# Kernel optimization log

Hardware: AMD Instinct MI355X
Metric: run time of the kernel (lower is better)

## Reference

```python
import jax, jax.numpy as jnp
import numpy as np

HIDDEN = 128
IN = 28
OUT = 28


def _uniform(key, shape, fan_in):
    bound = 1.0 / np.sqrt(fan_in)
    return jax.random.uniform(key, shape, jnp.float32, -bound, bound)


def setup_inputs() -> dict:
    key = jax.random.key(0)
    ks = jax.random.split(key, 8)
    B, T = 4096, 256
    x = jax.random.normal(ks[0], (B, T, IN), jnp.float32)
    hidden = jnp.zeros((B, HIDDEN), jnp.float32)
    # torch nn.Linear default init: U(-1/sqrt(fan_in), 1/sqrt(fan_in))
    W_ih = _uniform(ks[1], (HIDDEN, IN), IN)
    b_ih = _uniform(ks[2], (HIDDEN,), IN)
    W_hh = _uniform(ks[3], (HIDDEN, HIDDEN), HIDDEN)
    b_hh = _uniform(ks[4], (HIDDEN,), HIDDEN)
    W_ho = _uniform(ks[5], (OUT * OUT, HIDDEN), HIDDEN)
    b_ho = _uniform(ks[6], (OUT * OUT,), HIDDEN)
    return {"x": x, "hidden": hidden, "W_ih": W_ih, "b_ih": b_ih,
            "W_hh": W_hh, "b_hh": b_hh, "W_ho": W_ho, "b_ho": b_ho}


def reference(x, hidden, W_ih, b_ih, W_hh, b_hh, W_ho, b_ho):
    # x: [B, T, IN]; hidden: [B, HIDDEN]
    def step(h, x_t):
        h = jax.nn.relu(x_t @ W_ih.T + b_ih + h @ W_hh.T + b_hh)
        return h, None

    # scan over time (leading axis) — equivalent to the python loop,
    # and only the final hidden feeds the output projection (the torch
    # code overwrites `output` every step, so only the last one matters).
    h_final, _ = jax.lax.scan(step, hidden, jnp.swapaxes(x, 0, 1))
    out = (h_final @ W_ho.T + b_ho).reshape(-1, OUT, OUT)  # [B, 28, 28]
    return out, h_final
```

## Files before the change

### kernel.cpp

```cpp
#include <hip/hip_runtime.h>
#include <hip/hip_bf16.h>

#define B_TOT   4096
#define T_STEPS 256
#define IN_D    28
#define HID     128
#define OUT_D   784
#define BM      16

typedef __bf16 bf16x8 __attribute__((ext_vector_type(8)));
typedef __bf16 bf16x4 __attribute__((ext_vector_type(4)));
typedef float  f32x4  __attribute__((ext_vector_type(4)));
typedef float  f32x2  __attribute__((ext_vector_type(2)));

__device__ __forceinline__ float bf2f(__bf16 b) {
    unsigned short s = __builtin_bit_cast(unsigned short, b);
    unsigned int u = ((unsigned int)s) << 16;
    return __builtin_bit_cast(float, u);
}
__device__ __forceinline__ unsigned short f2bfbits(float f) {
    unsigned int u = __builtin_bit_cast(unsigned int, f);
    u += 0x7fffu + ((u >> 16) & 1u);
    return (unsigned short)(u >> 16);
}

__device__ __forceinline__ int hswz(int row, int byteInRow) {
    return row * 256 + (byteInRow ^ ((row & 7) << 4));
}

#define BARLDS() asm volatile("s_waitcnt lgkmcnt(0)\n\ts_barrier" ::: "memory")

__global__ __launch_bounds__(512) void rnn_fused(
    const float* __restrict__ x,
    const float* __restrict__ h0,
    const float* __restrict__ W_ih,
    const float* __restrict__ b_ih,
    const float* __restrict__ W_hh,
    const float* __restrict__ b_hh,
    const float* __restrict__ W_ho,
    const float* __restrict__ b_ho,
    float* __restrict__ out)
{
    __shared__ __align__(16) unsigned char Hb[2][BM * 256];
    __shared__ __align__(16) unsigned char Xs[8 * BM * 256];

    const int tid  = threadIdx.x;
    const int lane = tid & 63;
    const int wv   = tid >> 6;
    const int ln15 = lane & 15;
    const int lg   = lane >> 4;
    const int b0   = blockIdx.x * BM;

    const int nt0 = wv * 16;
    bf16x8 bw[4];
    #pragma unroll
    for (int kc = 0; kc < 4; ++kc) {
        const float* p = W_hh + (nt0 + ln15) * HID + kc * 32 + lg * 8;
        bf16x8 v;
        #pragma unroll
        for (int e = 0; e < 8; ++e) v[e] = (__bf16)p[e];
        bw[kc] = v;
    }
    const __bf16 bzero = (__bf16)0.0f;
    bf16x8 bxf;
    {
        int n = nt0 + ln15;
        #pragma unroll
        for (int e = 0; e < 8; ++e) {
            int k = lg * 8 + e;
            bxf[e] = (k < IN_D) ? (__bf16)W_ih[n * IN_D + k] : bzero;
        }
    }
    f32x4 bias4;
    {
        int n = nt0 + 4 * lg;
        f32x4 bi = *(const f32x4*)(b_ih + n);
        f32x4 bh = *(const f32x4*)(b_hh + n);
        bias4 = bi + bh;
    }

    if (tid < 256) {
        int row = tid >> 4, cg = tid & 15;
        const float* p = h0 + (size_t)(b0 + row) * HID + cg * 8;
        bf16x8 hv;
        #pragma unroll
        for (int e = 0; e < 8; ++e) hv[e] = (__bf16)p[e];
        *(bf16x8*)(&Hb[0][hswz(row, cg * 16)]) = hv;
    }
    if (tid < 256) {
        int slot = tid >> 5, idx = tid & 31, row = idx >> 1, d = idx & 1;
        *(unsigned int*)(&Xs[slot * (BM * 256) + hswz(row, 56 + d * 4)]) = 0u;
    }
    const int xrow = tid / 14, xpair = tid % 14;
    const bool xthr = (tid < 224);
    const float* xbase = x + (size_t)(b0 + xrow) * T_STEPS * IN_D + xpair * 2;
    if (xthr) {
        #pragma unroll
        for (int s = 0; s < 4; ++s) {
            f32x2 v = *(const f32x2*)(xbase + (size_t)s * IN_D);
            unsigned int pk = ((unsigned int)f2bfbits(v[1]) << 16) | f2bfbits(v[0]);
            *(unsigned int*)(&Xs[s * (BM * 256) + hswz(xrow, xpair * 4)]) = pk;
        }
    }
    f32x2 sx0 = {0.f, 0.f}, sx1 = sx0, sx2 = sx0, sx3 = sx0;
    __syncthreads();

#define STEP(T, STGL, STGW)                                                     \
    {                                                                           \
        const int rb = (T) & 1;                                                 \
        STGL                                                                    \
        bf16x8 ax  = *(const bf16x8*)(&Xs[((T) & 7) * (BM * 256) + hswz(ln15, lg * 16)]); \
        bf16x8 ah0 = *(const bf16x8*)(&Hb[rb][hswz(ln15,   0 + lg * 16)]);      \
        bf16x8 ah1 = *(const bf16x8*)(&Hb[rb][hswz(ln15,  64 + lg * 16)]);      \
        bf16x8 ah2 = *(const bf16x8*)(&Hb[rb][hswz(ln15, 128 + lg * 16)]);      \
        bf16x8 ah3 = *(const bf16x8*)(&Hb[rb][hswz(ln15, 192 + lg * 16)]);      \
        f32x4 zz = {0.f, 0.f, 0.f, 0.f};                                        \
        f32x4 a = __builtin_amdgcn_mfma_f32_16x16x32_bf16(bxf,   ax,  bias4, 0, 0, 0); \
        f32x4 c = __builtin_amdgcn_mfma_f32_16x16x32_bf16(bw[1], ah1, zz, 0, 0, 0); \
        a = __builtin_amdgcn_mfma_f32_16x16x32_bf16(bw[0], ah0, a, 0, 0, 0);    \
        c = __builtin_amdgcn_mfma_f32_16x16x32_bf16(bw[3], ah3, c, 0, 0, 0);    \
        a = __builtin_amdgcn_mfma_f32_16x16x32_bf16(bw[2], ah2, a, 0, 0, 0);    \
        f32x4 s = a + c;                                                        \
        bf16x4 w;                                                               \
        _Pragma("unroll")                                                       \
        for (int r = 0; r < 4; ++r) {                                           \
            float v = s[r];                                                     \
            w[r] = (__bf16)(v > 0.f ? v : 0.f);                                 \
        }                                                                       \
        *(bf16x4*)(&Hb[rb ^ 1][hswz(ln15, nt0 * 2 + lg * 8)]) = w;              \
        STGW                                                                    \
        BARLDS();                                                               \
    }

#define STG_LOAD(T)                                                             \
        if (((T) + 4 < T_STEPS) && xthr) {                                      \
            sx0 = *(const f32x2*)(xbase + (size_t)((T) + 4) * IN_D);            \
            sx1 = *(const f32x2*)(xbase + (size_t)((T) + 5) * IN_D);            \
            sx2 = *(const f32x2*)(xbase + (size_t)((T) + 6) * IN_D);            \
            sx3 = *(const f32x2*)(xbase + (size_t)((T) + 7) * IN_D);            \
        }
#define STG_WRITE(T)                                                            \
        if (((T) + 4 < T_STEPS) && xthr) {                                      \
            unsigned int p0 = ((unsigned int)f2bfbits(sx0[1]) << 16) | f2bfbits(sx0[0]); \
            unsigned int p1 = ((unsigned int)f2bfbits(sx1[1]) << 16) | f2bfbits(sx1[0]); \
            unsigned int p2 = ((unsigned int)f2bfbits(sx2[1]) << 16) | f2bfbits(sx2[0]); \
            unsigned int p3 = ((unsigned int)f2bfbits(sx3[1]) << 16) | f2bfbits(sx3[0]); \
            *(unsigned int*)(&Xs[(((T) + 4) & 7) * (BM * 256) + hswz(xrow, xpair * 4)]) = p0; \
            *(unsigned int*)(&Xs[(((T) + 5) & 7) * (BM * 256) + hswz(xrow, xpair * 4)]) = p1; \
            *(unsigned int*)(&Xs[(((T) + 6) & 7) * (BM * 256) + hswz(xrow, xpair * 4)]) = p2; \
            *(unsigned int*)(&Xs[(((T) + 7) & 7) * (BM * 256) + hswz(xrow, xpair * 4)]) = p3; \
        }

    for (int t = 0; t < T_STEPS; t += 8) {
        STEP(t + 0, STG_LOAD(t + 0), )
        STEP(t + 1, , )
        STEP(t + 2, , STG_WRITE(t + 0))
        STEP(t + 3, , )
        STEP(t + 4, STG_LOAD(t + 4), )
        STEP(t + 5, , )
        STEP(t + 6, , STG_WRITE(t + 4))
        STEP(t + 7, , )
    }
#undef STEP
#undef STG_LOAD
#undef STG_WRITE

    if (tid < 256) {
        int row = tid >> 4, cg = tid & 15;
        bf16x8 hv = *(const bf16x8*)(&Hb[0][hswz(row, cg * 16)]);
        float* po = out + (size_t)B_TOT * OUT_D + (size_t)(b0 + row) * HID + cg * 8;
        #pragma unroll
        for (int e = 0; e < 8; ++e) po[e] = bf2f(hv[e]);
    }
    bf16x8 af[4];
    #pragma unroll
    for (int kc = 0; kc < 4; ++kc)
        af[kc] = *(const bf16x8*)(&Hb[0][hswz(ln15, kc * 64 + lg * 16)]);

    for (int nt = wv; nt < 49; nt += 8) {
        f32x4 acc = *(const f32x4*)(b_ho + nt * 16 + 4 * lg);
        #pragma unroll
        for (int kc = 0; kc < 4; ++kc) {
            const float* p = W_ho + (nt * 16 + ln15) * HID + kc * 32 + lg * 8;
            bf16x8 bfrag;
            #pragma unroll
            for (int e = 0; e < 8; ++e) bfrag[e] = (__bf16)p[e];
            acc = __builtin_amdgcn_mfma_f32_16x16x32_bf16(bfrag, af[kc], acc, 0, 0, 0);
        }
        *(f32x4*)(out + (size_t)(b0 + ln15) * OUT_D + nt * 16 + 4 * lg) = acc;
    }
}

extern "C" void kernel_launch(void* const* d_in, const int* in_sizes, int n_in,
                              void* d_out, int out_size, void* d_ws, size_t ws_size,
                              hipStream_t stream) {
    const float* x    = (const float*)d_in[0];
    const float* h0   = (const float*)d_in[1];
    const float* W_ih = (const float*)d_in[2];
    const float* b_ih = (const float*)d_in[3];
    const float* W_hh = (const float*)d_in[4];
    const float* b_hh = (const float*)d_in[5];
    const float* W_ho = (const float*)d_in[6];
    const float* b_ho = (const float*)d_in[7];
    rnn_fused<<<B_TOT / BM, 512, 0, stream>>>(x, h0, W_ih, b_ih, W_hh, b_hh,
                                              W_ho, b_ho, (float*)d_out);
}
```

Measured before the change: 86.34 us.

## Batch input projections for eight steps off the recurrent critical path

Each group of eight timesteps now computes all eight input-projection MFMAs up front, from the full 8-slot X staging buffer. This takes the x@W_ih MFMA out of the serial h-dependency chain, leaving four MFMAs per step on that chain. The global-to-LDS staging is reorganized to prefetch a full group of eight steps ahead, and the prologue now fills all eight slots. The cost is eight more live accumulator vectors, which raises register pressure, and a burst of eight MFMAs at step 0 of each group.

```diff
diff --git a/kernel.cpp b/kernel.cpp
--- a/kernel.cpp
+++ b/kernel.cpp
@@ -96,7 +96,7 @@
     const float* xbase = x + (size_t)(b0 + xrow) * T_STEPS * IN_D + xpair * 2;
     if (xthr) {
         #pragma unroll
-        for (int s = 0; s < 4; ++s) {
+        for (int s = 0; s < 8; ++s) {
             f32x2 v = *(const f32x2*)(xbase + (size_t)s * IN_D);
             unsigned int pk = ((unsigned int)f2bfbits(v[1]) << 16) | f2bfbits(v[0]);
             *(unsigned int*)(&Xs[s * (BM * 256) + hswz(xrow, xpair * 4)]) = pk;
@@ -105,21 +105,42 @@
     f32x2 sx0 = {0.f, 0.f}, sx1 = sx0, sx2 = sx0, sx3 = sx0;
     __syncthreads();
 
-#define STEP(T, STGL, STGW)                                                     \
+    f32x4 u0, u1, u2, u3, u4, u5, u6, u7;
+
+#define PRE8(T)                                                                 \
+        {                                                                       \
+            bf16x8 ax0 = *(const bf16x8*)(&Xs[0 * (BM * 256) + hswz(ln15, lg * 16)]); \
+            bf16x8 ax1 = *(const bf16x8*)(&Xs[1 * (BM * 256) + hswz(ln15, lg * 16)]); \
+            bf16x8 ax2 = *(const bf16x8*)(&Xs[2 * (BM * 256) + hswz(ln15, lg * 16)]); \
+            bf16x8 ax3 = *(const bf16x8*)(&Xs[3 * (BM * 256) + hswz(ln15, lg * 16)]); \
+            bf16x8 ax4 = *(const bf16x8*)(&Xs[4 * (BM * 256) + hswz(ln15, lg * 16)]); \
+            bf16x8 ax5 = *(const bf16x8*)(&Xs[5 * (BM * 256) + hswz(ln15, lg * 16)]); \
+            bf16x8 ax6 = *(const bf16x8*)(&Xs[6 * (BM * 256) + hswz(ln15, lg * 16)]); \
+            bf16x8 ax7 = *(const bf16x8*)(&Xs[7 * (BM * 256) + hswz(ln15, lg * 16)]); \
+            u0 = __builtin_amdgcn_mfma_f32_16x16x32_bf16(bxf, ax0, bias4, 0, 0, 0); \
+            u1 = __builtin_amdgcn_mfma_f32_16x16x32_bf16(bxf, ax1, bias4, 0, 0, 0); \
+            u2 = __builtin_amdgcn_mfma_f32_16x16x32_bf16(bxf, ax2, bias4, 0, 0, 0); \
+            u3 = __builtin_amdgcn_mfma_f32_16x16x32_bf16(bxf, ax3, bias4, 0, 0, 0); \
+            u4 = __builtin_amdgcn_mfma_f32_16x16x32_bf16(bxf, ax4, bias4, 0, 0, 0); \
+            u5 = __builtin_amdgcn_mfma_f32_16x16x32_bf16(bxf, ax5, bias4, 0, 0, 0); \
+            u6 = __builtin_amdgcn_mfma_f32_16x16x32_bf16(bxf, ax6, bias4, 0, 0, 0); \
+            u7 = __builtin_amdgcn_mfma_f32_16x16x32_bf16(bxf, ax7, bias4, 0, 0, 0); \
+        }
+
+#define STEP(T, U, PRE, STGL, STGW)                                             \
     {                                                                           \
         const int rb = (T) & 1;                                                 \
+        PRE                                                                     \
         STGL                                                                    \
-        bf16x8 ax  = *(const bf16x8*)(&Xs[((T) & 7) * (BM * 256) + hswz(ln15, lg * 16)]); \
         bf16x8 ah0 = *(const bf16x8*)(&Hb[rb][hswz(ln15,   0 + lg * 16)]);      \
         bf16x8 ah1 = *(const bf16x8*)(&Hb[rb][hswz(ln15,  64 + lg * 16)]);      \
         bf16x8 ah2 = *(const bf16x8*)(&Hb[rb][hswz(ln15, 128 + lg * 16)]);      \
         bf16x8 ah3 = *(const bf16x8*)(&Hb[rb][hswz(ln15, 192 + lg * 16)]);      \
         f32x4 zz = {0.f, 0.f, 0.f, 0.f};                                        \
-        f32x4 a = __builtin_amdgcn_mfma_f32_16x16x32_bf16(bxf,   ax,  bias4, 0, 0, 0); \
+        f32x4 a = __builtin_amdgcn_mfma_f32_16x16x32_bf16(bw[0], ah0, U, 0, 0, 0); \
         f32x4 c = __builtin_amdgcn_mfma_f32_16x16x32_bf16(bw[1], ah1, zz, 0, 0, 0); \
-        a = __builtin_amdgcn_mfma_f32_16x16x32_bf16(bw[0], ah0, a, 0, 0, 0);    \
+        a = __builtin_amdgcn_mfma_f32_16x16x32_bf16(bw[2], ah2, a, 0, 0, 0);    \
         c = __builtin_amdgcn_mfma_f32_16x16x32_bf16(bw[3], ah3, c, 0, 0, 0);    \
-        a = __builtin_amdgcn_mfma_f32_16x16x32_bf16(bw[2], ah2, a, 0, 0, 0);    \
         f32x4 s = a + c;                                                        \
         bf16x4 w;                                                               \
         _Pragma("unroll")                                                       \
@@ -132,36 +153,37 @@
         BARLDS();                                                               \
     }
 
-#define STG_LOAD(T)                                                             \
-        if (((T) + 4 < T_STEPS) && xthr) {                                      \
-            sx0 = *(const f32x2*)(xbase + (size_t)((T) + 4) * IN_D);            \
-            sx1 = *(const f32x2*)(xbase + (size_t)((T) + 5) * IN_D);            \
-            sx2 = *(const f32x2*)(xbase + (size_t)((T) + 6) * IN_D);            \
-            sx3 = *(const f32x2*)(xbase + (size_t)((T) + 7) * IN_D);            \
-        }
-#define STG_WRITE(T)                                                            \
-        if (((T) + 4 < T_STEPS) && xthr) {                                      \
+#define STG_LOAD(TF)                                                            \
+        if (((TF) < T_STEPS) && xthr) {                                         \
+            sx0 = *(const f32x2*)(xbase + (size_t)((TF) + 0) * IN_D);           \
+            sx1 = *(const f32x2*)(xbase + (size_t)((TF) + 1) * IN_D);           \
+            sx2 = *(const f32x2*)(xbase + (size_t)((TF) + 2) * IN_D);           \
+            sx3 = *(const f32x2*)(xbase + (size_t)((TF) + 3) * IN_D);           \
+        }
+#define STG_WRITE(TF)                                                           \
+        if (((TF) < T_STEPS) && xthr) {                                         \
             unsigned int p0 = ((unsigned int)f2bfbits(sx0[1]) << 16) | f2bfbits(sx0[0]); \
             unsigned int p1 = ((unsigned int)f2bfbits(sx1[1]) << 16) | f2bfbits(sx1[0]); \
             unsigned int p2 = ((unsigned int)f2bfbits(sx2[1]) << 16) | f2bfbits(sx2[0]); \
             unsigned int p3 = ((unsigned int)f2bfbits(sx3[1]) << 16) | f2bfbits(sx3[0]); \
-            *(unsigned int*)(&Xs[(((T) + 4) & 7) * (BM * 256) + hswz(xrow, xpair * 4)]) = p0; \
-            *(unsigned int*)(&Xs[(((T) + 5) & 7) * (BM * 256) + hswz(xrow, xpair * 4)]) = p1; \
-            *(unsigned int*)(&Xs[(((T) + 6) & 7) * (BM * 256) + hswz(xrow, xpair * 4)]) = p2; \
-            *(unsigned int*)(&Xs[(((T) + 7) & 7) * (BM * 256) + hswz(xrow, xpair * 4)]) = p3; \
+            *(unsigned int*)(&Xs[(((TF) + 0) & 7) * (BM * 256) + hswz(xrow, xpair * 4)]) = p0; \
+            *(unsigned int*)(&Xs[(((TF) + 1) & 7) * (BM * 256) + hswz(xrow, xpair * 4)]) = p1; \
+            *(unsigned int*)(&Xs[(((TF) + 2) & 7) * (BM * 256) + hswz(xrow, xpair * 4)]) = p2; \
+            *(unsigned int*)(&Xs[(((TF) + 3) & 7) * (BM * 256) + hswz(xrow, xpair * 4)]) = p3; \
         }
 
     for (int t = 0; t < T_STEPS; t += 8) {
-        STEP(t + 0, STG_LOAD(t + 0), )
-        STEP(t + 1, , )
-        STEP(t + 2, , STG_WRITE(t + 0))
-        STEP(t + 3, , )
-        STEP(t + 4, STG_LOAD(t + 4), )
-        STEP(t + 5, , )
-        STEP(t + 6, , STG_WRITE(t + 4))
-        STEP(t + 7, , )
+        STEP(t + 0, u0, PRE8(t), , )
+        STEP(t + 1, u1, , STG_LOAD(t + 8), )
+        STEP(t + 2, u2, , , )
+        STEP(t + 3, u3, , , )
+        STEP(t + 4, u4, , , STG_WRITE(t + 8))
+        STEP(t + 5, u5, , STG_LOAD(t + 12), )
+        STEP(t + 6, u6, , , )
+        STEP(t + 7, u7, , , STG_WRITE(t + 12))
     }
 #undef STEP
+#undef PRE8
 #undef STG_LOAD
 #undef STG_WRITE
 
```

Result: no change. 84.77 us (median of 2 runs) (-1.8%).
